# Optimization experiments

Measured on AMD Instinct MI355X. Metric: run time of the kernel, lower is better.

Reference implementation:

```python
import jax, jax.numpy as jnp
import numpy as np

N = 50000
F = 256
E = 800000


def setup_inputs() -> dict:
    key = jax.random.key(0)
    k1, k2, k3, k4 = jax.random.split(key, 4)
    H = jax.random.normal(k1, (N, F), dtype=jnp.float32)
    H0 = jax.random.normal(k2, (N, F), dtype=jnp.float32)
    # edge list for sparse adjacency: row 0 = i (row index), row 1 = j (col index)
    edge_index = jax.random.randint(k3, (2, E), 0, N, dtype=jnp.int32)
    # W ~ U(-stdv, stdv), stdv = 1/sqrt(out_features), as in reset_parameters
    stdv = 1.0 / np.sqrt(F)
    W = jax.random.uniform(k4, (F, F), minval=-stdv, maxval=stdv, dtype=jnp.float32)
    lamda = jnp.float32(0.5)
    alpha = jnp.float32(0.1)
    l = 4
    return {"H": H, "edge_index": edge_index, "H0": H0, "W": W,
            "lamda": lamda, "alpha": alpha, "l": l}


def reference(H, edge_index, H0, W, lamda, alpha, l):
    n = H.shape[0]
    src = edge_index[0]  # i: row index of A[i, j]
    dst = edge_index[1]  # j: col index
    # A_hat = A + I ; degree = column sums of A_hat (tf.reduce_sum(A_hat, 0))
    deg = jax.ops.segment_sum(jnp.ones(src.shape[0], dtype=H.dtype), dst,
                              num_segments=n) + 1.0
    d_inv_sqrt = jax.lax.rsqrt(deg)
    # (P H)_i = d_i^{-1/2} * sum_j A[i,j] d_j^{-1/2} H_j  +  H_i / d_i  (self loop)
    msg = H[dst] * d_inv_sqrt[dst][:, None]            # [E, F]
    agg = jax.ops.segment_sum(msg, src, num_segments=n)  # [N, F]
    PH = d_inv_sqrt[:, None] * agg + H / deg[:, None]
    init_res = (1.0 - alpha) * PH + alpha * H0
    beta = jnp.log(lamda / l + 1.0)
    # init_res @ ((1-beta) I + beta W)
    output = (1.0 - beta) * init_res + beta * (init_res @ W)
    return output
```

## Files before the change

kernel.cpp:

```cpp
#include <hip/hip_runtime.h>
#include <math.h>


#define F_DIM 256
#define CHUNK 10000

typedef __attribute__((ext_vector_type(4))) float f32x4;
typedef __attribute__((ext_vector_type(8))) short short8;
typedef __attribute__((ext_vector_type(4))) unsigned short u16x4;

static __device__ __forceinline__ unsigned short f2bf(float f) {
    unsigned int u = __float_as_uint(f);
    u += 0x7fffu + ((u >> 16) & 1u);
    return (unsigned short)(u >> 16);
}
static __device__ __forceinline__ float bf2f(unsigned short u) {
    return __uint_as_float((unsigned int)u << 16);
}


__global__ __launch_bounds__(1024) void hist_kernel(
        const int* __restrict__ src, const int* __restrict__ dst,
        unsigned* __restrict__ histS, unsigned* __restrict__ histD,
        unsigned short* __restrict__ lrank, int E, int wpc, int whalf) {
    __shared__ unsigned hist[12544];
    int b = blockIdx.x;
    int which = b & 1, h = (b >> 1) & 1, c = b >> 2;
    int tid = threadIdx.x;
    int w0 = h * whalf;
    int hcount = h ? (wpc - whalf) : whalf;
    int e0 = c * CHUNK;
    int e1 = e0 + CHUNK < E ? e0 + CHUNK : E;
    const int* eptr = which ? dst : src;
    unsigned* outh = which ? histD : histS;

    for (int w = tid; w < hcount; w += 1024) hist[w] = 0;
    __syncthreads();
    for (int e = e0 + tid; e < e1; e += 1024) {
        int s = eptr[e];
        int wl = (s >> 1) - w0;
        if ((unsigned)wl < (unsigned)hcount) {
            int sh = (s & 1) * 16;
            unsigned old = atomicAdd(&hist[wl], 1u << sh);
            if (!which) lrank[e] = (unsigned short)((old >> sh) & 0xffffu);
        }
    }
    __syncthreads();
    for (int w = tid; w < hcount; w += 1024)
        outh[(size_t)c * wpc + w0 + w] = hist[w];
}


__global__ __launch_bounds__(256) void sumbase_kernel(
        const unsigned* __restrict__ histS, const unsigned* __restrict__ histD,
        int* __restrict__ cnt, float* __restrict__ dinv,
        unsigned* __restrict__ baseL, int* __restrict__ blksum,
        int wpc, int nchunk, int n) {
    int tid = threadIdx.x;
    int w = blockIdx.x * 256 + tid;
    size_t stride2 = (size_t)2 * wpc;
    unsigned slo = 0, shi = 0, dlo = 0, dhi = 0;
    if (w < wpc) {
        for (int c = 0; c < nchunk; ++c) {
            unsigned vs = histS[(size_t)c * wpc + w];
            unsigned vd = histD[(size_t)c * wpc + w];
            baseL[c * stride2 + 2 * w]     = slo;
            baseL[c * stride2 + 2 * w + 1] = shi;
            slo += vs & 0xffffu; shi += vs >> 16;
            dlo += vd & 0xffffu; dhi += vd >> 16;
        }
        int i0 = 2 * w, i1 = 2 * w + 1;
        cnt[i0] = (int)slo;
        dinv[i0] = rsqrtf((float)dlo + 1.0f);
        if (i1 < n) {
            cnt[i1] = (int)shi;
            dinv[i1] = rsqrtf((float)dhi + 1.0f);
        }
    }
    int contrib = 0;
    if (w < wpc) {
        contrib = (int)slo;
        if (2 * w + 1 < n) contrib += (int)shi;
    }
    int lane = tid & 63, wid = tid >> 6;
    int v = contrib;
    for (int off = 32; off > 0; off >>= 1) v += __shfl_down(v, off, 64);
    __shared__ int ws4[4];
    if (lane == 0) ws4[wid] = v;
    __syncthreads();
    if (tid == 0)   blksum[2 * blockIdx.x]     = ws4[0] + ws4[1];
    if (tid == 128) blksum[2 * blockIdx.x + 1] = ws4[2] + ws4[3];
}


__global__ __launch_bounds__(256) void blkscan_kernel(const int* __restrict__ blksum,
                                                      int* __restrict__ blkoff, int nb) {
    int tid = threadIdx.x;
    int v = (tid < nb) ? blksum[tid] : 0;
    int s = v;
    int lane = tid & 63, w = tid >> 6;
    for (int off = 1; off < 64; off <<= 1) {
        int t = __shfl_up(v, off, 64);
        if (lane >= off) v += t;
    }
    __shared__ int ws[4];
    if (lane == 63) ws[w] = v;
    __syncthreads();
    if (tid == 0) {
        int run = 0;
        for (int i = 0; i < 4; ++i) { int t = ws[i]; ws[i] = run; run += t; }
    }
    __syncthreads();
    if (tid < nb) blkoff[tid] = ws[w] + v - s;
}

__global__ __launch_bounds__(256) void rowptr_kernel(const int* __restrict__ cnt,
                                                     const int* __restrict__ blkoff,
                                                     int* __restrict__ row_ptr, int n) {
    int i = blockIdx.x * 256 + threadIdx.x;
    int tid = threadIdx.x;
    int s = (i < n) ? cnt[i] : 0;
    int v = s;
    int lane = tid & 63, w = tid >> 6;
    for (int off = 1; off < 64; off <<= 1) {
        int t = __shfl_up(v, off, 64);
        if (lane >= off) v += t;
    }
    __shared__ int ws[4];
    if (lane == 63) ws[w] = v;
    __syncthreads();
    if (tid == 0) {
        int run = 0;
        for (int k = 0; k < 4; ++k) { int t = ws[k]; ws[k] = run; run += t; }
    }
    __syncthreads();
    if (i <= n) row_ptr[i] = blkoff[blockIdx.x] + ws[w] + v - s;
}


__global__ __launch_bounds__(256) void fill_kernel(
        const int* __restrict__ src, const int* __restrict__ dst,
        const int* __restrict__ row_ptr, const unsigned* __restrict__ baseL,
        const unsigned short* __restrict__ lrank,
        int* __restrict__ col, int E, int wpc) {
    int e = blockIdx.x * 256 + threadIdx.x;
    if (e < E) {
        int c = e / CHUNK;
        int s = src[e];
        unsigned pos = (unsigned)row_ptr[s] + baseL[(size_t)c * (2 * wpc) + s]
                     + lrank[e];
        col[pos] = dst[e];
    }
}


__global__ __launch_bounds__(256) void hswt_kernel(const float* __restrict__ H,
                                                   const float* __restrict__ dinv,
                                                   unsigned short* __restrict__ Hs,
                                                   const float* __restrict__ W,
                                                   unsigned short* __restrict__ Wt,
                                                   const float* __restrict__ lamda_p,
                                                   const int* __restrict__ l_p,
                                                   int total4) {
    int i = blockIdx.x * 256 + threadIdx.x;
    if (i < total4) {
        int row = i >> 6;
        float d = dinv[row];
        f32x4 x = ((const f32x4*)H)[i];
        u16x4 o;
        o[0] = f2bf(x[0] * d); o[1] = f2bf(x[1] * d);
        o[2] = f2bf(x[2] * d); o[3] = f2bf(x[3] * d);
        ((u16x4*)Hs)[i] = o;
    } else {
        int t = i - total4;
        if (t < F_DIM * F_DIM) {
            float beta = logf(lamda_p[0] / (float)l_p[0] + 1.0f);
            int nn = t >> 8, kk = t & 255;
            float v = beta * W[kk * F_DIM + nn];
            if (kk == nn) v += 1.0f - beta;
            Wt[nn * F_DIM + kk] = f2bf(v);
        }
    }
}


#define ACC(A, h) { A[0] += bf2f(h[0]); A[1] += bf2f(h[1]); \
                    A[2] += bf2f(h[2]); A[3] += bf2f(h[3]); }

__global__ __launch_bounds__(256) void gather_kernel(
        const unsigned short* __restrict__ Hs, const float* __restrict__ H0,
        const int* __restrict__ row_ptr, const int* __restrict__ col,
        const float* __restrict__ dinv, const float* __restrict__ alpha_p,
        unsigned short* __restrict__ irb, int n) {
    int wave = threadIdx.x >> 6;
    int lane = threadIdx.x & 63;
    int row = blockIdx.x * 4 + wave;
    if (row >= n) return;
    float alpha = alpha_p[0];
    const u16x4* Hs4 = (const u16x4*)Hs;

    int beg = row_ptr[row], end = row_ptr[row + 1];
    f32x4 a0 = 0.0f, a1 = 0.0f, a2 = 0.0f, a3 = 0.0f;
    int e = beg;
    for (; e + 8 <= end; e += 8) {
        int j0 = col[e+0], j1 = col[e+1], j2 = col[e+2], j3 = col[e+3];
        int j4 = col[e+4], j5 = col[e+5], j6 = col[e+6], j7 = col[e+7];
        u16x4 h0 = Hs4[j0*64+lane], h1 = Hs4[j1*64+lane];
        u16x4 h2 = Hs4[j2*64+lane], h3 = Hs4[j3*64+lane];
        u16x4 h4 = Hs4[j4*64+lane], h5 = Hs4[j5*64+lane];
        u16x4 h6 = Hs4[j6*64+lane], h7 = Hs4[j7*64+lane];
        ACC(a0, h0) ACC(a1, h1) ACC(a2, h2) ACC(a3, h3)
        ACC(a0, h4) ACC(a1, h5) ACC(a2, h6) ACC(a3, h7)
    }
    for (; e + 4 <= end; e += 4) {
        int j0 = col[e+0], j1 = col[e+1], j2 = col[e+2], j3 = col[e+3];
        u16x4 h0 = Hs4[j0*64+lane], h1 = Hs4[j1*64+lane];
        u16x4 h2 = Hs4[j2*64+lane], h3 = Hs4[j3*64+lane];
        ACC(a0, h0) ACC(a1, h1) ACC(a2, h2) ACC(a3, h3)
    }
    for (; e < end; ++e) {
        int j = col[e];
        u16x4 h = Hs4[j*64+lane];
        ACC(a0, h)
    }
    u16x4 hr = Hs4[row*64+lane];
    ACC(a2, hr)
    f32x4 acc = (a0 + a1) + (a2 + a3);
    float di = dinv[row];
    f32x4 h0v = ((const f32x4*)H0)[row * 64 + lane];
    f32x4 init = (1.0f - alpha) * (di * acc) + alpha * h0v;
    u16x4 o;
    o[0] = f2bf(init[0]); o[1] = f2bf(init[1]);
    o[2] = f2bf(init[2]); o[3] = f2bf(init[3]);
    ((u16x4*)irb)[row * 64 + lane] = o;
}


__global__ __launch_bounds__(256) void gemm_kernel(
        const unsigned short* __restrict__ irb, const unsigned short* __restrict__ Wt,
        float* __restrict__ out, int M) {
    int w = threadIdx.x >> 6;
    int mr = blockIdx.x * 64;
    int nc = w * 64;
    int lane = threadIdx.x & 63;
    int lo = lane & 15, hi = lane >> 4;

    f32x4 acc[4][4] = {};
    for (int kk = 0; kk < 8; ++kk) {
        int kb = kk * 32 + hi * 8;
        short8 a[4], b[4];
        for (int am = 0; am < 4; ++am) {
            int row = mr + am * 16 + lo;
            a[am] = (row < M) ? *(const short8*)(irb + (size_t)row * F_DIM + kb)
                              : (short8)0;
        }
        for (int bn = 0; bn < 4; ++bn) {
            int cb = nc + bn * 16 + lo;
            b[bn] = *(const short8*)(Wt + cb * F_DIM + kb);
        }
        for (int am = 0; am < 4; ++am)
            for (int bn = 0; bn < 4; ++bn)
                acc[am][bn] = __builtin_amdgcn_mfma_f32_16x16x32_bf16(
                    a[am], b[bn], acc[am][bn], 0, 0, 0);
    }

    for (int am = 0; am < 4; ++am) {
        int rbase = mr + am * 16 + hi * 4;
        for (int r = 0; r < 4; ++r) {
            int row = rbase + r;
            if (row >= M) continue;
            for (int bn = 0; bn < 4; ++bn) {
                int c2 = nc + bn * 16 + lo;
                out[(size_t)row * F_DIM + c2] = acc[am][bn][r];
            }
        }
    }
}


extern "C" void kernel_launch(void* const* d_in, const int* in_sizes, int n_in,
                              void* d_out, int out_size, void* d_ws, size_t ws_size,
                              hipStream_t stream) {
    const float* H     = (const float*)d_in[0];
    const int*   ei    = (const int*)d_in[1];
    const float* H0    = (const float*)d_in[2];
    const float* W     = (const float*)d_in[3];
    const float* lamda = (const float*)d_in[4];
    const float* alpha = (const float*)d_in[5];
    const int*   lp    = (const int*)d_in[6];

    int n = in_sizes[0] / F_DIM;
    int E = in_sizes[1] / 2;
    const int* src = ei;
    const int* dst = ei + E;
    float* out = (float*)d_out;

    int wpc = (n + 1) / 2;
    int whalf = (wpc + 1) / 2;
    int nchunk = (E + CHUNK - 1) / CHUNK;
    int nb = (n + 256) / 256;

    char* ws = (char*)d_ws;
    size_t off = 0;
    auto alloc = [&](size_t bytes) -> void* {
        void* p = ws + off;
        off += (bytes + 255) & ~(size_t)255;
        return p;
    };
    unsigned* histS = (unsigned*)alloc((size_t)nchunk * wpc * 4);
    unsigned* histD = (unsigned*)alloc((size_t)nchunk * wpc * 4);
    unsigned* baseL = (unsigned*)alloc((size_t)nchunk * 2 * wpc * 4);
    unsigned short* lrank = (unsigned short*)alloc((size_t)E * 2);
    int* cnt     = (int*)alloc((size_t)n * 4);
    int* row_ptr = (int*)alloc(((size_t)n + 1) * 4);
    int* blksum  = (int*)alloc((size_t)(2 * ((wpc + 255) / 256) + 8) * 4);
    int* blkoff  = (int*)alloc((size_t)nb * 4);
    float* dinv  = (float*)alloc((size_t)n * 4);
    int* colb    = (int*)alloc((size_t)E * 4);
    unsigned short* Wt  = (unsigned short*)alloc((size_t)F_DIM * F_DIM * 2);
    unsigned short* Hs  = (unsigned short*)alloc((size_t)n * F_DIM * 2);
    unsigned short* irb = (unsigned short*)alloc(((size_t)n + 64) * F_DIM * 2);

    hist_kernel<<<nchunk * 4, 1024, 0, stream>>>(src, dst, histS, histD, lrank,
                                                 E, wpc, whalf);
    int wgrid = (wpc + 255) / 256;
    sumbase_kernel<<<wgrid, 256, 0, stream>>>(histS, histD, cnt, dinv, baseL,
                                              blksum, wpc, nchunk, n);
    blkscan_kernel<<<1, 256, 0, stream>>>(blksum, blkoff, nb);
    rowptr_kernel<<<nb, 256, 0, stream>>>(cnt, blkoff, row_ptr, n);
    fill_kernel<<<(E + 255) / 256, 256, 0, stream>>>(src, dst, row_ptr, baseL,
                                                     lrank, colb, E, wpc);
    int total4 = n * 64;
    int hswt_items = total4 + F_DIM * F_DIM;
    hswt_kernel<<<(hswt_items + 255) / 256, 256, 0, stream>>>(H, dinv, Hs, W, Wt,
                                                              lamda, lp, total4);
    gather_kernel<<<(n + 3) / 4, 256, 0, stream>>>(Hs, H0, row_ptr, colb, dinv,
                                                   alpha, irb, n);
    int mtiles = (n + 63) / 64;
    gemm_kernel<<<mtiles, 256, 0, stream>>>(irb, Wt, out, n);
}
```

Measured before the change: 180.8 us.

## Fuse CSR build launches, pack per-chunk base offsets, and enlarge edge chunks

Folds the block-offset scan into the row-pointer kernel, so every block rescans the block sums itself and one launch disappears. The fill (CSR column scatter) and the H-scaling/W-transpose kernels are merged into a single grid that splits work by block index. Per-chunk base offsets are packed as two 16-bit values per word, halving that buffer. CHUNK is doubled to halve the histogram and base arrays and the serial loop in sumbase. The aim is fewer launches and less traffic, but the 16-bit packing of cumulative base offsets assumes no node has 65536 or more edges as a source within prior chunks.

Result: faster. 162.1 us (-10.3%).

```diff
diff --git a/kernel.cpp b/kernel.cpp
--- a/kernel.cpp
+++ b/kernel.cpp
@@ -3,7 +3,7 @@
 
 
 #define F_DIM 256
-#define CHUNK 10000
+#define CHUNK 20000
 
 typedef __attribute__((ext_vector_type(4))) float f32x4;
 typedef __attribute__((ext_vector_type(8))) short short8;
@@ -58,14 +58,12 @@
         int wpc, int nchunk, int n) {
     int tid = threadIdx.x;
     int w = blockIdx.x * 256 + tid;
-    size_t stride2 = (size_t)2 * wpc;
     unsigned slo = 0, shi = 0, dlo = 0, dhi = 0;
     if (w < wpc) {
         for (int c = 0; c < nchunk; ++c) {
             unsigned vs = histS[(size_t)c * wpc + w];
             unsigned vd = histD[(size_t)c * wpc + w];
-            baseL[c * stride2 + 2 * w]     = slo;
-            baseL[c * stride2 + 2 * w + 1] = shi;
+            baseL[(size_t)c * wpc + w] = slo | (shi << 16);
             slo += vs & 0xffffu; shi += vs >> 16;
             dlo += vd & 0xffffu; dhi += vd >> 16;
         }
@@ -93,12 +91,33 @@
 }
 
 
-__global__ __launch_bounds__(256) void blkscan_kernel(const int* __restrict__ blksum,
-                                                      int* __restrict__ blkoff, int nb) {
+__global__ __launch_bounds__(256) void rowptr_kernel(const int* __restrict__ cnt,
+                                                     const int* __restrict__ blksum,
+                                                     int* __restrict__ row_ptr,
+                                                     int n, int nb) {
     int tid = threadIdx.x;
-    int v = (tid < nb) ? blksum[tid] : 0;
-    int s = v;
     int lane = tid & 63, w = tid >> 6;
+    int bv = (tid < nb) ? blksum[tid] : 0;
+    int bs = bv;
+    for (int off = 1; off < 64; off <<= 1) {
+        int t = __shfl_up(bv, off, 64);
+        if (lane >= off) bv += t;
+    }
+    __shared__ int wsb[4];
+    __shared__ int sbo[256];
+    if (lane == 63) wsb[w] = bv;
+    __syncthreads();
+    if (tid == 0) {
+        int run = 0;
+        for (int k = 0; k < 4; ++k) { int t = wsb[k]; wsb[k] = run; run += t; }
+    }
+    __syncthreads();
+    sbo[tid] = wsb[w] + bv - bs;
+    __syncthreads();
+    int blockoff = sbo[blockIdx.x];
+    int i = blockIdx.x * 256 + tid;
+    int s = (i < n) ? cnt[i] : 0;
+    int v = s;
     for (int off = 1; off < 64; off <<= 1) {
         int t = __shfl_up(v, off, 64);
         if (lane >= off) v += t;
@@ -108,77 +127,53 @@
     __syncthreads();
     if (tid == 0) {
         int run = 0;
-        for (int i = 0; i < 4; ++i) { int t = ws[i]; ws[i] = run; run += t; }
-    }
-    __syncthreads();
-    if (tid < nb) blkoff[tid] = ws[w] + v - s;
-}
-
-__global__ __launch_bounds__(256) void rowptr_kernel(const int* __restrict__ cnt,
-                                                     const int* __restrict__ blkoff,
-                                                     int* __restrict__ row_ptr, int n) {
-    int i = blockIdx.x * 256 + threadIdx.x;
-    int tid = threadIdx.x;
-    int s = (i < n) ? cnt[i] : 0;
-    int v = s;
-    int lane = tid & 63, w = tid >> 6;
-    for (int off = 1; off < 64; off <<= 1) {
-        int t = __shfl_up(v, off, 64);
-        if (lane >= off) v += t;
-    }
-    __shared__ int ws[4];
-    if (lane == 63) ws[w] = v;
-    __syncthreads();
-    if (tid == 0) {
-        int run = 0;
         for (int k = 0; k < 4; ++k) { int t = ws[k]; ws[k] = run; run += t; }
     }
     __syncthreads();
-    if (i <= n) row_ptr[i] = blkoff[blockIdx.x] + ws[w] + v - s;
-}
-
-
-__global__ __launch_bounds__(256) void fill_kernel(
+    if (i <= n) row_ptr[i] = blockoff + ws[w] + v - s;
+}
+
+
+__global__ __launch_bounds__(256) void fillhswt_kernel(
         const int* __restrict__ src, const int* __restrict__ dst,
         const int* __restrict__ row_ptr, const unsigned* __restrict__ baseL,
-        const unsigned short* __restrict__ lrank,
-        int* __restrict__ col, int E, int wpc) {
-    int e = blockIdx.x * 256 + threadIdx.x;
-    if (e < E) {
-        int c = e / CHUNK;
-        int s = src[e];
-        unsigned pos = (unsigned)row_ptr[s] + baseL[(size_t)c * (2 * wpc) + s]
-                     + lrank[e];
-        col[pos] = dst[e];
-    }
-}
-
-
-__global__ __launch_bounds__(256) void hswt_kernel(const float* __restrict__ H,
-                                                   const float* __restrict__ dinv,
-                                                   unsigned short* __restrict__ Hs,
-                                                   const float* __restrict__ W,
-                                                   unsigned short* __restrict__ Wt,
-                                                   const float* __restrict__ lamda_p,
-                                                   const int* __restrict__ l_p,
-                                                   int total4) {
-    int i = blockIdx.x * 256 + threadIdx.x;
-    if (i < total4) {
-        int row = i >> 6;
-        float d = dinv[row];
-        f32x4 x = ((const f32x4*)H)[i];
-        u16x4 o;
-        o[0] = f2bf(x[0] * d); o[1] = f2bf(x[1] * d);
-        o[2] = f2bf(x[2] * d); o[3] = f2bf(x[3] * d);
-        ((u16x4*)Hs)[i] = o;
+        const unsigned short* __restrict__ lrank, int* __restrict__ col,
+        const float* __restrict__ H, const float* __restrict__ dinv,
+        unsigned short* __restrict__ Hs,
+        const float* __restrict__ W, unsigned short* __restrict__ Wt,
+        const float* __restrict__ lamda_p, const int* __restrict__ l_p,
+        int E, int wpc, int nfill, int total4) {
+    int bid = blockIdx.x;
+    int tid = threadIdx.x;
+    if (bid < nfill) {
+        int e = bid * 256 + tid;
+        if (e < E) {
+            int c = e / CHUNK;
+            int s = src[e];
+            unsigned word = baseL[(size_t)c * wpc + (s >> 1)];
+            unsigned lb = (s & 1) ? (word >> 16) : (word & 0xffffu);
+            unsigned pos = (unsigned)row_ptr[s] + lb + lrank[e];
+            col[pos] = dst[e];
+        }
     } else {
-        int t = i - total4;
-        if (t < F_DIM * F_DIM) {
-            float beta = logf(lamda_p[0] / (float)l_p[0] + 1.0f);
-            int nn = t >> 8, kk = t & 255;
-            float v = beta * W[kk * F_DIM + nn];
-            if (kk == nn) v += 1.0f - beta;
-            Wt[nn * F_DIM + kk] = f2bf(v);
+        int i = (bid - nfill) * 256 + tid;
+        if (i < total4) {
+            int row = i >> 6;
+            float d = dinv[row];
+            f32x4 x = ((const f32x4*)H)[i];
+            u16x4 o;
+            o[0] = f2bf(x[0] * d); o[1] = f2bf(x[1] * d);
+            o[2] = f2bf(x[2] * d); o[3] = f2bf(x[3] * d);
+            ((u16x4*)Hs)[i] = o;
+        } else {
+            int t = i - total4;
+            if (t < F_DIM * F_DIM) {
+                float beta = logf(lamda_p[0] / (float)l_p[0] + 1.0f);
+                int nn = t >> 8, kk = t & 255;
+                float v = beta * W[kk * F_DIM + nn];
+                if (kk == nn) v += 1.0f - beta;
+                Wt[nn * F_DIM + kk] = f2bf(v);
+            }
         }
     }
 }
@@ -309,12 +304,11 @@
     };
     unsigned* histS = (unsigned*)alloc((size_t)nchunk * wpc * 4);
     unsigned* histD = (unsigned*)alloc((size_t)nchunk * wpc * 4);
-    unsigned* baseL = (unsigned*)alloc((size_t)nchunk * 2 * wpc * 4);
+    unsigned* baseL = (unsigned*)alloc((size_t)nchunk * wpc * 4);
     unsigned short* lrank = (unsigned short*)alloc((size_t)E * 2);
     int* cnt     = (int*)alloc((size_t)n * 4);
     int* row_ptr = (int*)alloc(((size_t)n + 1) * 4);
-    int* blksum  = (int*)alloc((size_t)(2 * ((wpc + 255) / 256) + 8) * 4);
-    int* blkoff  = (int*)alloc((size_t)nb * 4);
+    int* blksum  = (int*)alloc((size_t)(nb + 8) * 4);
     float* dinv  = (float*)alloc((size_t)n * 4);
     int* colb    = (int*)alloc((size_t)E * 4);
     unsigned short* Wt  = (unsigned short*)alloc((size_t)F_DIM * F_DIM * 2);
@@ -326,14 +320,13 @@
     int wgrid = (wpc + 255) / 256;
     sumbase_kernel<<<wgrid, 256, 0, stream>>>(histS, histD, cnt, dinv, baseL,
                                               blksum, wpc, nchunk, n);
-    blkscan_kernel<<<1, 256, 0, stream>>>(blksum, blkoff, nb);
-    rowptr_kernel<<<nb, 256, 0, stream>>>(cnt, blkoff, row_ptr, n);
-    fill_kernel<<<(E + 255) / 256, 256, 0, stream>>>(src, dst, row_ptr, baseL,
-                                                     lrank, colb, E, wpc);
+    rowptr_kernel<<<nb, 256, 0, stream>>>(cnt, blksum, row_ptr, n, nb);
+    int nfill = (E + 255) / 256;
     int total4 = n * 64;
-    int hswt_items = total4 + F_DIM * F_DIM;
-    hswt_kernel<<<(hswt_items + 255) / 256, 256, 0, stream>>>(H, dinv, Hs, W, Wt,
-                                                              lamda, lp, total4);
+    int nhswt = (total4 + F_DIM * F_DIM + 255) / 256;
+    fillhswt_kernel<<<nfill + nhswt, 256, 0, stream>>>(
+        src, dst, row_ptr, baseL, lrank, colb,
+        H, dinv, Hs, W, Wt, lamda, lp, E, wpc, nfill, total4);
     gather_kernel<<<(n + 3) / 4, 256, 0, stream>>>(Hs, H0, row_ptr, colb, dinv,
                                                    alpha, irb, n);
     int mtiles = (n + 63) / 64;
```
